# Performance work log

Hardware: AMD Instinct MI355X
Metric: run time of the kernel (lower is better)

Reference implementation:

```python
import jax, jax.numpy as jnp
import numpy as np

EPS = 1e-5
CURVE_LEN = 16


def gather_neighbors(feature, idx):
    # feature: [B, C, N], idx: [B, N, k] -> [B, C, N, k]
    return jax.vmap(lambda f, i: f[:, i])(feature, idx)


def cloud_walk(feature, knn_idx):
    # feature: [B, C, N], knn_idx: [B, N, k] -> walk_index [B, N, 16] (int)
    B, C, N = feature.shape
    neigh = gather_neighbors(feature, knn_idx)                 # [B, C, N, k]
    sim = jnp.einsum('bcn,bcnk->bnk', feature, neigh)          # [B, N, k]
    attn = jax.nn.softmax(sim, axis=-1)
    top4 = jax.lax.top_k(attn, 4)[1]                           # [B, N, 4]
    tmp = top4.reshape(B * N, 4)
    nxt = top4[:, :, 1]                                        # [B, N]
    walks = [nxt]
    for _ in range(CURVE_LEN - 1):
        # faithful to original: index rows of tmp by previous step's values
        nxt = tmp[nxt.reshape(-1), 1].reshape(B, N)
        walks.append(nxt)
    return jnp.stack(walks, axis=-1)                           # [B, N, 16]


def self_attention_layer(feature, walk_idx, Wq, bq, Wk, bk, Wv, bv, gamma, beta):
    # feature: [B, C, N], walk_idx: [B, N, 16]
    wf = gather_neighbors(feature, walk_idx)                   # [B, C, N, 16]
    wf = jnp.transpose(wf, (0, 2, 3, 1))                       # [B, N, 16, C]
    center = jnp.transpose(feature, (0, 2, 1))[:, :, None, :]  # [B, N, 1, C]
    win = jnp.concatenate([wf, center], axis=2)                # [B, N, 17, C]
    Q = win @ Wq.T + bq
    K = win @ Wk.T + bk
    V = win @ Wv.T + bv
    sim = jnp.einsum('bnic,bnjc->bnij', Q, K)                  # [B, N, 17, 17]
    attn = jax.nn.softmax(sim, axis=-1)
    # original einsum 'bnkk,bnkc->bnc' => diagonal of attention weights V
    d = jnp.diagonal(attn, axis1=2, axis2=3)                   # [B, N, 17]
    out = jnp.einsum('bnk,bnkc->bnc', d, V)                    # [B, N, C]
    x = jnp.transpose(out, (0, 2, 1))                          # [B, C, N]
    # BatchNorm1d, training mode: stats over (batch, points), biased variance
    mean = jnp.mean(x, axis=(0, 2), keepdims=True)
    var = jnp.mean((x - mean) ** 2, axis=(0, 2), keepdims=True)
    x = gamma[None, :, None] * (x - mean) / jnp.sqrt(var + EPS) + beta[None, :, None]
    x = jax.nn.relu(x)
    return feature + x


def setup_inputs() -> dict:
    key = jax.random.key(0)
    B, C, N, k = 2, 64, 32768, 16
    ks = jax.random.split(key, 10)
    feature = jax.random.normal(ks[0], (B, C, N), dtype=jnp.float32)
    knn_idx = jax.random.randint(ks[1], (B, N, k), 0, N)
    Wq = jax.random.normal(ks[2], (3, C, C), dtype=jnp.float32) * 0.05
    bq = jax.random.normal(ks[3], (3, C), dtype=jnp.float32) * 0.05
    Wk = jax.random.normal(ks[4], (3, C, C), dtype=jnp.float32) * 0.05
    bk = jax.random.normal(ks[5], (3, C), dtype=jnp.float32) * 0.05
    Wv = jax.random.normal(ks[6], (3, C, C), dtype=jnp.float32) * 0.05
    bv = jax.random.normal(ks[7], (3, C), dtype=jnp.float32) * 0.05
    gamma = jnp.ones((3, C), dtype=jnp.float32)
    beta = jnp.zeros((3, C), dtype=jnp.float32)
    return {"feature": feature, "knn_idx": knn_idx, "Wq": Wq, "bq": bq,
            "Wk": Wk, "bk": bk, "Wv": Wv, "bv": bv, "gamma": gamma, "beta": beta}


def reference(feature, knn_idx, Wq, bq, Wk, bk, Wv, bv, gamma, beta):
    walk_idx = cloud_walk(feature, knn_idx)
    heads = []
    f = feature
    for i in range(3):
        f = self_attention_layer(f, walk_idx, Wq[i], bq[i], Wk[i], bk[i],
                                 Wv[i], bv[i], gamma[i], beta[i])
        heads.append(f)
    return jnp.concatenate(heads, axis=1)  # [B, 3C, N]
```

## Files before the change

kernel.cpp:

```cpp
#include <hip/hip_runtime.h>
#include <math.h>

#define NB 2
#define NC 64
#define NN 32768
#define NPTS (NB*NN)
#define NWAVES 1056
#define NSLOTS 67584

typedef _Float16 half_t;
typedef _Float16 f16x8 __attribute__((ext_vector_type(8)));
typedef _Float16 f16x4 __attribute__((ext_vector_type(4)));
typedef float f32x4 __attribute__((ext_vector_type(4)));

__global__ void k_transpose(const float* __restrict__ f, float* __restrict__ fT,
                            half_t* __restrict__ xh) {
    int blk = blockIdx.x;
    int b = blk / (NN/64);
    int n0 = (blk % (NN/64)) * 64;
    __shared__ float tile[64][65];
    int t = threadIdx.x;
    int dn = t & 63, c0 = t >> 6;
    for (int i = 0; i < 16; ++i) {
        int c = c0 + i*4;
        tile[c][dn] = f[((size_t)(b*NC + c))*NN + n0 + dn];
    }
    __syncthreads();
    int o = t & 63, d0 = t >> 6;
    for (int i = 0; i < 16; ++i) {
        int dn2 = d0 + i*4;
        size_t idx = ((size_t)(b*NN + n0 + dn2))*64 + o;
        float v = tile[o][dn2];
        fT[idx] = v;
        xh[idx] = (half_t)v;
    }
}

__global__ __launch_bounds__(256, 4) void k_s2(const float* __restrict__ fT,
                                               const int* __restrict__ knn,
                                               int* __restrict__ s2buf) {
    int t = threadIdx.x;
    int gp = blockIdx.x * 16 + (t >> 4);
    int l16 = t & 15;
    int q4 = l16 & 3;
    int h4 = l16 >> 2;
    int b = gp >> 15;
    const float4* cen4 = (const float4*)(fT + (size_t)gp*64 + q4*16);
    float4 c0 = cen4[0], c1 = cen4[1], c2 = cen4[2], c3 = cen4[3];
    float own[4];
    #pragma unroll
    for (int kk = 0; kk < 4; ++kk) {
        int idx = knn[(gp << 4) + h4*4 + kk];
        const float4* nb = (const float4*)(fT + ((size_t)(b*NN + idx))*64 + q4*16);
        float4 n0 = nb[0], n1 = nb[1], n2 = nb[2], n3 = nb[3];
        double a = 0.0;
        a += (double)c0.x*(double)n0.x + (double)c0.y*(double)n0.y
           + (double)c0.z*(double)n0.z + (double)c0.w*(double)n0.w;
        a += (double)c1.x*(double)n1.x + (double)c1.y*(double)n1.y
           + (double)c1.z*(double)n1.z + (double)c1.w*(double)n1.w;
        a += (double)c2.x*(double)n2.x + (double)c2.y*(double)n2.y
           + (double)c2.z*(double)n2.z + (double)c2.w*(double)n2.w;
        a += (double)c3.x*(double)n3.x + (double)c3.y*(double)n3.y
           + (double)c3.z*(double)n3.z + (double)c3.w*(double)n3.w;
        a += __shfl_xor(a, 1, 64);
        a += __shfl_xor(a, 2, 64);
        own[kk] = (float)a;
    }
    int base16 = t & 48;
    float sims[16];
    #pragma unroll
    for (int j = 0; j < 16; ++j)
        sims[j] = __shfl(own[j & 3], base16 + ((j >> 2) << 2), 64);
    float m = sims[0];
    #pragma unroll
    for (int k = 1; k < 16; ++k) m = fmaxf(m, sims[k]);
    float e[16]; float Z = 0.f;
    #pragma unroll
    for (int k = 0; k < 16; ++k) { e[k] = expf(sims[k]-m); Z += e[k]; }
    float b1 = -1.f, b2 = -1.f; int i1 = -1, i2 = -1;
    #pragma unroll
    for (int k = 0; k < 16; ++k) {
        float a = e[k]/Z;
        if (a > b1)      { b2 = b1; i2 = i1; b1 = a; i1 = k; }
        else if (a > b2) { b2 = a; i2 = k; }
    }
    if (l16 == 0) s2buf[gp] = i2;
}

__global__ void k_hist2(const int* __restrict__ s2buf, int* __restrict__ bh) {
    __shared__ int hst[32];
    int t = threadIdx.x, blk = blockIdx.x;
    if (t < 32) hst[t] = 0;
    __syncthreads();
    int p = blk*256 + t;
    int bucket = (p >> 15)*16 + s2buf[p];
    atomicAdd(&hst[bucket], 1);
    __syncthreads();
    if (t < 32) bh[t*256 + blk] = hst[t];
}

__global__ void k_prefix(const int* __restrict__ s2buf, const int* __restrict__ bh,
                         int* __restrict__ blockoff, int* __restrict__ wavebucket,
                         int* __restrict__ slotlist, int* __restrict__ walkrows) {
    __shared__ int tot[32], wst[32], offsh;
    __shared__ int T[16];
    int t = threadIdx.x;
    if (t < 16) T[t] = s2buf[t];
    if (t < 32) {
        int s = 0;
        for (int b = 0; b < 256; ++b) s += bh[t*256 + b];
        tot[t] = s;
    }
    __syncthreads();
    if (t < 16) {
        int w = t;
        walkrows[t*16 + 0] = w;
        for (int s = 1; s < 16; ++s) { w = T[w]; walkrows[t*16 + s] = w; }
    }
    if (t == 0) {
        int off = 0;
        for (int i = 0; i < 32; ++i) {
            wst[i] = off;
            off += ((tot[i] + 63) >> 6) << 6;
        }
        offsh = off;
    }
    __syncthreads();
    if (t < 32) {
        int run = wst[t];
        for (int b = 0; b < 256; ++b) {
            blockoff[t*256 + b] = run;
            run += bh[t*256 + b];
        }
        int w0 = wst[t] >> 6, nw = (tot[t] + 63) >> 6;
        for (int w = 0; w < nw; ++w) wavebucket[w0 + w] = t;
        for (int s = wst[t] + tot[t]; s < wst[t] + nw*64; ++s) slotlist[s] = -1;
    }
    __syncthreads();
    int off = offsh;
    for (int w = (off >> 6) + t; w < NWAVES; w += 256) wavebucket[w] = -1;
    for (int s = off + t; s < NSLOTS; s += 256) slotlist[s] = -1;
}

__global__ void k_scatter2(const int* __restrict__ s2buf,
                           const int* __restrict__ blockoff,
                           int* __restrict__ slotlist) {
    __shared__ int hst[32], base[32];
    int t = threadIdx.x, blk = blockIdx.x;
    if (t < 32) { hst[t] = 0; base[t] = blockoff[t*256 + blk]; }
    __syncthreads();
    int p = blk*256 + t;
    int bucket = (p >> 15)*16 + s2buf[p];
    int r = atomicAdd(&hst[bucket], 1);
    slotlist[base[bucket] + r] = p;
}

__global__ __launch_bounds__(256) void k_precomp(
        const float* __restrict__ fT,
        const float* __restrict__ Wq, const float* __restrict__ bq,
        const float* __restrict__ Wk, const float* __restrict__ bk,
        const float* __restrict__ Wv, const float* __restrict__ bv,
        const int* __restrict__ walkrows,
        half_t* __restrict__ Pq16, half_t* __restrict__ Pk16,
        half_t* __restrict__ PvT16, float* __restrict__ Pstat,
        half_t* __restrict__ wh) {
    int blk = blockIdx.x;
    int b = blk >> 4, sv = blk & 15;
    size_t bsv16 = (size_t)(b*16 + sv) * 1024;
    int bs48 = (b*16 + sv)*48;
    __shared__ float win[16][64];
    __shared__ float Wl[64][65];
    __shared__ float qw[16][65], kw[16][65];
    __shared__ float simw[16][17];
    __shared__ int wr[16];
    int t = threadIdx.x;
    #pragma unroll
    for (int j = 0; j < 2; ++j) {
        int idx = j*8192 + blk*256 + t;
        if (idx < 12288) {
            float v = idx < 4096 ? Wq[idx] : (idx < 8192 ? Wk[idx-4096] : Wv[idx-8192]);
            wh[idx] = (half_t)v;
        }
    }
    if (t < 16) wr[t] = walkrows[sv*16 + t];
    __syncthreads();
    #pragma unroll
    for (int i = 0; i < 4; ++i) {
        int idx = t + i*256; int tt = idx >> 6, c = idx & 63;
        win[tt][c] = fT[((size_t)(b*NN + wr[tt]))*64 + c];
    }
    int wv = t >> 6, lane = t & 63;
    for (int m = 0; m < 3; ++m) {
        const float* W  = m == 0 ? Wq : (m == 1 ? Wk : Wv);
        const float* bb = m == 0 ? bq : (m == 1 ? bk : bv);
        __syncthreads();
        #pragma unroll
        for (int i = 0; i < 16; ++i) {
            int idx = t + i*256;
            Wl[idx >> 6][idx & 63] = W[idx];
        }
        __syncthreads();
        float acc[4] = {0.f, 0.f, 0.f, 0.f};
        for (int c = 0; c < 64; ++c) {
            float w_ = Wl[lane][c];
            #pragma unroll
            for (int r = 0; r < 4; ++r) acc[r] = fmaf(w_, win[wv*4 + r][c], acc[r]);
        }
        float bias = bb[lane];
        #pragma unroll
        for (int r = 0; r < 4; ++r) {
            int tt = wv*4 + r;
            float val = acc[r] + bias;
            if (m == 0)      { qw[tt][lane] = val; Pq16[bsv16 + tt*64 + lane] = (half_t)val; }
            else if (m == 1) { kw[tt][lane] = val; Pk16[bsv16 + tt*64 + lane] = (half_t)val; }
            else             {                     PvT16[bsv16 + lane*16 + tt] = (half_t)val; }
        }
    }
    __syncthreads();
    {
        int i = t >> 4, j = t & 15;
        float acc = 0.f;
        for (int o = 0; o < 64; ++o) acc = fmaf(qw[i][o], kw[j][o], acc);
        simw[i][j] = acc;
    }
    __syncthreads();
    if (t < 16) {
        float mx = simw[t][0];
        for (int j = 1; j < 16; ++j) mx = fmaxf(mx, simw[t][j]);
        float z = 0.f;
        for (int j = 0; j < 16; ++j) z += expf(simw[t][j] - mx);
        Pstat[bs48 + t*3 + 0] = mx;
        Pstat[bs48 + t*3 + 1] = z;
        Pstat[bs48 + t*3 + 2] = simw[t][t];
    }
}

__global__ __launch_bounds__(256) void k_gemm(
        const half_t* __restrict__ xh, const int* __restrict__ slotlist, int s0,
        const half_t* __restrict__ wh,
        const float* __restrict__ bq, const float* __restrict__ bk,
        const float* __restrict__ bv,
        half_t* __restrict__ qh, half_t* __restrict__ kh, half_t* __restrict__ vh) {
    __shared__ __align__(16) half_t XO[256*72];
    __shared__ __align__(16) half_t WL[192*72];
    int t = threadIdx.x;
    int lane = t & 63, wv = t >> 6;
    size_t go = (size_t)blockIdx.x * 256 * 64;
    {
        int srow = slotlist[s0 + blockIdx.x*256 + t];
        int prow = srow < 0 ? 0 : srow;
        const uint4* src = (const uint4*)(xh + (size_t)prow*64);
        #pragma unroll
        for (int j = 0; j < 8; ++j) *(uint4*)&XO[t*72 + j*8] = src[j];
    }
    #pragma unroll
    for (int j = 0; j < 6; ++j) {
        int idx8 = t + j*256;
        int row = idx8 >> 3, c0 = (idx8 & 7) * 8;
        *(uint4*)&WL[row*72 + c0] = *(const uint4*)(wh + idx8*8);
    }
    __syncthreads();
    int m15 = lane & 15, k0 = (lane >> 4) * 8;
    int ar = wv*64 + m15;
    f16x8 a00 = *(const f16x8*)&XO[(ar    )*72 + k0];
    f16x8 a01 = *(const f16x8*)&XO[(ar    )*72 + k0 + 32];
    f16x8 a10 = *(const f16x8*)&XO[(ar+16)*72 + k0];
    f16x8 a11 = *(const f16x8*)&XO[(ar+16)*72 + k0 + 32];
    f16x8 a20 = *(const f16x8*)&XO[(ar+32)*72 + k0];
    f16x8 a21 = *(const f16x8*)&XO[(ar+32)*72 + k0 + 32];
    f16x8 a30 = *(const f16x8*)&XO[(ar+48)*72 + k0];
    f16x8 a31 = *(const f16x8*)&XO[(ar+48)*72 + k0 + 32];
    __syncthreads();
    #pragma unroll 1
    for (int m = 0; m < 3; ++m) {
        const float* bias = m == 0 ? bq : (m == 1 ? bk : bv);
        half_t* outp      = m == 0 ? qh : (m == 1 ? kh : vh);
        int wb = m*64 + m15;
        f16x8 b00 = *(const f16x8*)&WL[(wb    )*72 + k0];
        f16x8 b01 = *(const f16x8*)&WL[(wb    )*72 + k0 + 32];
        f16x8 b10 = *(const f16x8*)&WL[(wb+16)*72 + k0];
        f16x8 b11 = *(const f16x8*)&WL[(wb+16)*72 + k0 + 32];
        f16x8 b20 = *(const f16x8*)&WL[(wb+32)*72 + k0];
        f16x8 b21 = *(const f16x8*)&WL[(wb+32)*72 + k0 + 32];
        f16x8 b30 = *(const f16x8*)&WL[(wb+48)*72 + k0];
        f16x8 b31 = *(const f16x8*)&WL[(wb+48)*72 + k0 + 32];
        float bs0 = bias[m15], bs1 = bias[16+m15], bs2 = bias[32+m15], bs3 = bias[48+m15];
        f32x4 Z = {0.f, 0.f, 0.f, 0.f};
        f32x4 c00=Z,c01=Z,c02=Z,c03=Z, c10=Z,c11=Z,c12=Z,c13=Z;
        f32x4 c20=Z,c21=Z,c22=Z,c23=Z, c30=Z,c31=Z,c32=Z,c33=Z;
        #define MM(i,j) \
            c##i##j = __builtin_amdgcn_mfma_f32_16x16x32_f16(a##i##0, b##j##0, c##i##j, 0,0,0); \
            c##i##j = __builtin_amdgcn_mfma_f32_16x16x32_f16(a##i##1, b##j##1, c##i##j, 0,0,0);
        MM(0,0) MM(0,1) MM(0,2) MM(0,3)
        MM(1,0) MM(1,1) MM(1,2) MM(1,3)
        MM(2,0) MM(2,1) MM(2,2) MM(2,3)
        MM(3,0) MM(3,1) MM(3,2) MM(3,3)
        #undef MM
        __syncthreads();
        int r0 = wv*64 + ((lane >> 4) << 2);
        #define WR(i,j,bsj) { \
            XO[(r0 + i*16 + 0)*64 + j*16 + m15] = (half_t)(c##i##j[0] + bsj); \
            XO[(r0 + i*16 + 1)*64 + j*16 + m15] = (half_t)(c##i##j[1] + bsj); \
            XO[(r0 + i*16 + 2)*64 + j*16 + m15] = (half_t)(c##i##j[2] + bsj); \
            XO[(r0 + i*16 + 3)*64 + j*16 + m15] = (half_t)(c##i##j[3] + bsj); }
        WR(0,0,bs0) WR(0,1,bs1) WR(0,2,bs2) WR(0,3,bs3)
        WR(1,0,bs0) WR(1,1,bs1) WR(1,2,bs2) WR(1,3,bs3)
        WR(2,0,bs0) WR(2,1,bs1) WR(2,2,bs2) WR(2,3,bs3)
        WR(3,0,bs0) WR(3,1,bs1) WR(3,2,bs2) WR(3,3,bs3)
        #undef WR
        __syncthreads();
        #pragma unroll
        for (int j = 0; j < 8; ++j) {
            int idx = (j*256 + t) * 8;
            *(uint4*)(outp + go + idx) = *(const uint4*)&XO[idx];
        }
    }
}

__global__ __launch_bounds__(256) void k_comb4(
        const half_t* __restrict__ qh, const half_t* __restrict__ kh,
        const half_t* __restrict__ vh,
        const half_t* __restrict__ Pq16, const half_t* __restrict__ Pk16,
        const half_t* __restrict__ PvT16, const float* __restrict__ Pstat,
        const int* __restrict__ slotlist, const int* __restrict__ wavebucket,
        half_t* __restrict__ xo, int s0) {
    int t = threadIdx.x, j = t >> 6, lane = t & 63;
    int wslot = blockIdx.x*64;
    int gbase = s0 + wslot;
    int bucket = wavebucket[gbase >> 6];
    if (bucket < 0) return;
    int m15 = lane & 15, g4 = lane >> 4;
    int k0h = g4 * 8;
    size_t bsv16 = (size_t)bucket << 10;
    int bs48 = bucket * 48;

    f16x8 pqA0 = *(const f16x8*)&Pq16[bsv16 + m15*64 + k0h];
    f16x8 pqA1 = *(const f16x8*)&Pq16[bsv16 + m15*64 + k0h + 32];
    f16x8 pkA0 = *(const f16x8*)&Pk16[bsv16 + m15*64 + k0h];
    f16x8 pkA1 = *(const f16x8*)&Pk16[bsv16 + m15*64 + k0h + 32];
    f16x4 pvB0 = *(const f16x4*)&PvT16[bsv16 + (0*16 + m15)*16 + g4*4];
    f16x4 pvB1 = *(const f16x4*)&PvT16[bsv16 + (1*16 + m15)*16 + g4*4];
    f16x4 pvB2 = *(const f16x4*)&PvT16[bsv16 + (2*16 + m15)*16 + g4*4];
    f16x4 pvB3 = *(const f16x4*)&PvT16[bsv16 + (3*16 + m15)*16 + g4*4];
    float pm[4], pz[4], dg[4];
    #pragma unroll
    for (int r = 0; r < 4; ++r) {
        pm[r] = Pstat[bs48 + (g4*4+r)*3 + 0];
        pz[r] = Pstat[bs48 + (g4*4+r)*3 + 1];
        dg[r] = Pstat[bs48 + (g4*4+r)*3 + 2];
    }
    int4 pid4 = *(const int4*)&slotlist[gbase + j*16 + g4*4];

    const half_t* kp = kh + (size_t)(wslot + j*16 + m15)*64;
    const half_t* qp = qh + (size_t)(wslot + j*16 + m15)*64;
    f16x8 kB0 = *(const f16x8*)&kp[k0h];
    f16x8 kB1 = *(const f16x8*)&kp[k0h + 32];
    f16x8 qB0 = *(const f16x8*)&qp[k0h];
    f16x8 qB1 = *(const f16x8*)&qp[k0h + 32];
    f32x4 Zz = {0.f,0.f,0.f,0.f};
    f32x4 sp = __builtin_amdgcn_mfma_f32_16x16x32_f16(pqA0, kB0, Zz, 0,0,0);
    sp = __builtin_amdgcn_mfma_f32_16x16x32_f16(pqA1, kB1, sp, 0,0,0);
    f32x4 tp = __builtin_amdgcn_mfma_f32_16x16x32_f16(pkA0, qB0, Zz, 0,0,0);
    tp = __builtin_amdgcn_mfma_f32_16x16x32_f16(pkA1, qB1, tp, 0,0,0);
    float up = 0.f;
    #pragma unroll
    for (int e = 0; e < 8; ++e) {
        up = fmaf((float)qB0[e], (float)kB0[e], up);
        up = fmaf((float)qB1[e], (float)kB1[e], up);
    }
    up += __shfl_xor(up, 16, 64);
    up += __shfl_xor(up, 32, 64);
    float d0, d1, d2, d3;
    {
        float mi, zi;
        mi = fmaxf(pm[0], sp[0]); zi = pz[0]*expf(pm[0]-mi) + expf(sp[0]-mi); d0 = expf(dg[0]-mi)/zi;
        mi = fmaxf(pm[1], sp[1]); zi = pz[1]*expf(pm[1]-mi) + expf(sp[1]-mi); d1 = expf(dg[1]-mi)/zi;
        mi = fmaxf(pm[2], sp[2]); zi = pz[2]*expf(pm[2]-mi) + expf(sp[2]-mi); d2 = expf(dg[2]-mi)/zi;
        mi = fmaxf(pm[3], sp[3]); zi = pz[3]*expf(pm[3]-mi) + expf(sp[3]-mi); d3 = expf(dg[3]-mi)/zi;
    }
    float tmax = fmaxf(fmaxf(tp[0], tp[1]), fmaxf(tp[2], tp[3]));
    tmax = fmaxf(tmax, __shfl_xor(tmax, 16, 64));
    tmax = fmaxf(tmax, __shfl_xor(tmax, 32, 64));
    float mc = fmaxf(tmax, up);
    float ze = expf(tp[0]-mc) + expf(tp[1]-mc) + expf(tp[2]-mc) + expf(tp[3]-mc);
    ze += __shfl_xor(ze, 16, 64);
    ze += __shfl_xor(ze, 32, 64);
    float ec = expf(up - mc);
    float dcen = ec / (ze + ec);
    f16x4 dA; dA[0] = (half_t)d0; dA[1] = (half_t)d1; dA[2] = (half_t)d2; dA[3] = (half_t)d3;

    float dc0 = __shfl(dcen, g4*4 + 0, 64);
    float dc1 = __shfl(dcen, g4*4 + 1, 64);
    float dc2 = __shfl(dcen, g4*4 + 2, 64);
    float dc3 = __shfl(dcen, g4*4 + 3, 64);
    int p0 = pid4.x, p1 = pid4.y, p2 = pid4.z, p3 = pid4.w;
    size_t vb0 = (size_t)(wslot + j*16 + g4*4 + 0)*64;
    size_t vb1 = (size_t)(wslot + j*16 + g4*4 + 1)*64;
    size_t vb2 = (size_t)(wslot + j*16 + g4*4 + 2)*64;
    size_t vb3 = (size_t)(wslot + j*16 + g4*4 + 3)*64;
    #pragma unroll
    for (int jc = 0; jc < 4; ++jc) {
        f16x4 pvB = jc == 0 ? pvB0 : (jc == 1 ? pvB1 : (jc == 2 ? pvB2 : pvB3));
        f32x4 Z2 = {0.f,0.f,0.f,0.f};
        f32x4 acc = __builtin_amdgcn_mfma_f32_16x16x16f16(dA, pvB, Z2, 0,0,0);
        int c = jc*16 + m15;
        float v0 = (float)vh[vb0 + c];
        float v1 = (float)vh[vb1 + c];
        float v2 = (float)vh[vb2 + c];
        float v3 = (float)vh[vb3 + c];
        if (p0 >= 0) xo[(size_t)p0*64 + c] = (half_t)(acc[0] + dc0*v0);
        if (p1 >= 0) xo[(size_t)p1*64 + c] = (half_t)(acc[1] + dc1*v1);
        if (p2 >= 0) xo[(size_t)p2*64 + c] = (half_t)(acc[2] + dc2*v2);
        if (p3 >= 0) xo[(size_t)p3*64 + c] = (half_t)(acc[3] + dc3*v3);
    }
}

__global__ __launch_bounds__(256) void k_reduce(const half_t* __restrict__ x,
                                                float* __restrict__ part) {
    __shared__ float ls[4][64], lq[4][64];
    int t = threadIdx.x, q = t >> 6, c = t & 63;
    size_t base = ((size_t)blockIdx.x*128 + q*32) * 64;
    float s = 0.f, sq = 0.f;
    for (int r = 0; r < 32; ++r) {
        float v = (float)x[base + r*64 + c];
        s += v; sq = fmaf(v, v, sq);
    }
    ls[q][c] = s; lq[q][c] = sq;
    __syncthreads();
    if (q == 0) {
        float S = ls[0][c] + ls[1][c] + ls[2][c] + ls[3][c];
        float Q = lq[0][c] + lq[1][c] + lq[2][c] + lq[3][c];
        part[blockIdx.x*64 + c] = S;
        part[512*64 + blockIdx.x*64 + c] = Q;
    }
}

__global__ __launch_bounds__(256) void k_stats(const float* __restrict__ part,
                                               float* __restrict__ mv) {
    __shared__ float ls[4][64], lq[4][64];
    int t = threadIdx.x, q = t >> 6, c = t & 63;
    float s = 0.f, sq = 0.f;
    for (int r = q*128; r < q*128 + 128; ++r) {
        s  += part[r*64 + c];
        sq += part[512*64 + r*64 + c];
    }
    ls[q][c] = s; lq[q][c] = sq;
    __syncthreads();
    if (q == 0) {
        float S = ls[0][c] + ls[1][c] + ls[2][c] + ls[3][c];
        float Q = lq[0][c] + lq[1][c] + lq[2][c] + lq[3][c];
        float mean = S / (float)NPTS;
        float var  = Q / (float)NPTS - mean*mean;
        mv[c] = mean; mv[64 + c] = var;
    }
}

__global__ void k_norm(const half_t* __restrict__ x, float* __restrict__ fT,
                       const float* __restrict__ mv,
                       const float* __restrict__ gamma, const float* __restrict__ beta,
                       float* __restrict__ out, int l, half_t* __restrict__ xh) {
    int blk = blockIdx.x;
    int b = blk / (NN/64);
    int n0 = (blk % (NN/64)) * 64;
    __shared__ float tile[64][65];
    int t = threadIdx.x;
    int c = t & 63, d0 = t >> 6;
    float mean = mv[c], var = mv[64+c];
    float inv = 1.0f / sqrtf(var + 1e-5f);
    float ga = gamma[c], be = beta[c];
    for (int i = 0; i < 16; ++i) {
        int dn = d0 + i*4;
        size_t pi = ((size_t)(b*NN + n0 + dn))*64 + c;
        float xv = (float)x[pi];
        float y = fT[pi] + fmaxf(ga * (xv - mean) * inv + be, 0.f);
        fT[pi] = y;
        xh[pi] = (half_t)y;
        tile[dn][c] = y;
    }
    __syncthreads();
    int dn2 = t & 63, c0 = t >> 6;
    for (int i = 0; i < 16; ++i) {
        int cc = c0 + i*4;
        out[((size_t)(b*192 + l*64 + cc))*NN + n0 + dn2] = tile[dn2][cc];
    }
}

extern "C" void kernel_launch(void* const* d_in, const int* in_sizes, int n_in,
                              void* d_out, int out_size, void* d_ws, size_t ws_size,
                              hipStream_t stream) {
    const float* feature = (const float*)d_in[0];
    const int*   knn     = (const int*)d_in[1];
    const float* Wq = (const float*)d_in[2];
    const float* bq = (const float*)d_in[3];
    const float* Wk = (const float*)d_in[4];
    const float* bk = (const float*)d_in[5];
    const float* Wv = (const float*)d_in[6];
    const float* bv = (const float*)d_in[7];
    const float* gamma = (const float*)d_in[8];
    const float* beta  = (const float*)d_in[9];
    float* out = (float*)d_out;

    char* ws = (char*)d_ws;
    float*  fT    = (float*) ws;
    half_t* xh    = (half_t*)(ws + 16777216);
    half_t* xo    = (half_t*)(ws + 25165824);
    int*    s2buf = (int*)   (ws + 33554432);
    int*    walkrows = (int*)(ws + 33816576);
    half_t* Pq16  = (half_t*)(ws + 33817600);
    half_t* Pk16  = (half_t*)(ws + 33883136);
    half_t* PvT16 = (half_t*)(ws + 33948672);
    float*  Pstat = (float*) (ws + 34014208);
    float*  part  = (float*) (ws + 34020352);
    float*  mv    = (float*) (ws + 34282496);
    half_t* wh    = (half_t*)(ws + 34283008);
    int*    bh        = (int*)(ws + 34307584);
    int*    blockoff  = (int*)(ws + 34340352);
    int*    wavebucket= (int*)(ws + 34373120);
    int*    slotlist  = (int*)(ws + 34377344);
    size_t  qkv_off = 34647680;

    size_t avail = ws_size > qkv_off ? ws_size - qkv_off : 0;
    size_t chunk = avail / 384;
    chunk = (chunk / 256) * 256;
    if (chunk > (size_t)NSLOTS) chunk = NSLOTS;
    if (chunk < 256) chunk = 256;
    half_t* qh = (half_t*)(ws + qkv_off);
    half_t* kh = qh + chunk*64;
    half_t* vh = kh + chunk*64;

    k_transpose<<<NB*(NN/64), 256, 0, stream>>>(feature, fT, xh);
    k_s2<<<NPTS/16, 256, 0, stream>>>(fT, knn, s2buf);
    k_hist2<<<NPTS/256, 256, 0, stream>>>(s2buf, bh);
    k_prefix<<<1, 256, 0, stream>>>(s2buf, bh, blockoff, wavebucket, slotlist, walkrows);
    k_scatter2<<<NPTS/256, 256, 0, stream>>>(s2buf, blockoff, slotlist);

    for (int l = 0; l < 3; ++l) {
        k_precomp<<<32, 256, 0, stream>>>(fT, Wq + l*4096, bq + l*64,
                                          Wk + l*4096, bk + l*64,
                                          Wv + l*4096, bv + l*64,
                                          walkrows, Pq16, Pk16, PvT16, Pstat, wh);
        for (size_t s0 = 0; s0 < NSLOTS; s0 += chunk) {
            size_t cn = (s0 + chunk <= NSLOTS) ? chunk : (NSLOTS - s0);
            k_gemm<<<(unsigned)(cn/256), 256, 0, stream>>>(xh, slotlist, (int)s0, wh,
                                                           bq + l*64, bk + l*64, bv + l*64,
                                                           qh, kh, vh);
            k_comb4<<<(unsigned)(cn/64), 256, 0, stream>>>(qh, kh, vh,
                                                           Pq16, Pk16, PvT16, Pstat,
                                                           slotlist, wavebucket,
                                                           xo, (int)s0);
        }
        k_reduce<<<512, 256, 0, stream>>>(xo, part);
        k_stats<<<1, 256, 0, stream>>>(part, mv);
        k_norm<<<NB*(NN/64), 256, 0, stream>>>(xo, fT, mv, gamma + l*64, beta + l*64,
                                               out, l, xh);
    }
}
```

Measured before the change: 219.7 us.

## Fuse BN stats into reduce via last-block atomic and drop fp32 residual

Merges k_stats into the partial-sum reduction kernel: the last block to finish, found through an atomic counter, computes mean and variance, which removes three kernel launches. The residual stream is now kept only in fp16 (xh), so k_norm no longer reads and writes the fp32 fT buffer and k_precomp gathers from xh. This cuts memory traffic in k_norm but accumulates residual values in half precision across the three layers, which lowers accuracy. The counter is reset by the last block, which relies on threadfence ordering.

```diff
diff --git a/kernel.cpp b/kernel.cpp
--- a/kernel.cpp
+++ b/kernel.cpp
@@ -101,10 +101,12 @@
 
 __global__ void k_prefix(const int* __restrict__ s2buf, const int* __restrict__ bh,
                          int* __restrict__ blockoff, int* __restrict__ wavebucket,
-                         int* __restrict__ slotlist, int* __restrict__ walkrows) {
+                         int* __restrict__ slotlist, int* __restrict__ walkrows,
+                         int* __restrict__ cnt) {
     __shared__ int tot[32], wst[32], offsh;
     __shared__ int T[16];
     int t = threadIdx.x;
+    if (t == 0) *cnt = 0;
     if (t < 16) T[t] = s2buf[t];
     if (t < 32) {
         int s = 0;
@@ -156,7 +158,7 @@
 }
 
 __global__ __launch_bounds__(256) void k_precomp(
-        const float* __restrict__ fT,
+        const half_t* __restrict__ xh,
         const float* __restrict__ Wq, const float* __restrict__ bq,
         const float* __restrict__ Wk, const float* __restrict__ bk,
         const float* __restrict__ Wv, const float* __restrict__ bv,
@@ -187,7 +189,7 @@
     #pragma unroll
     for (int i = 0; i < 4; ++i) {
         int idx = t + i*256; int tt = idx >> 6, c = idx & 63;
-        win[tt][c] = fT[((size_t)(b*NN + wr[tt]))*64 + c];
+        win[tt][c] = (float)xh[((size_t)(b*NN + wr[tt]))*64 + c];
     }
     int wv = t >> 6, lane = t & 63;
     for (int m = 0; m < 3; ++m) {
@@ -415,9 +417,12 @@
     }
 }
 
-__global__ __launch_bounds__(256) void k_reduce(const half_t* __restrict__ x,
-                                                float* __restrict__ part) {
+__global__ __launch_bounds__(256) void k_reduce2(const half_t* __restrict__ x,
+                                                 float* __restrict__ part,
+                                                 float* __restrict__ mv,
+                                                 int* __restrict__ cnt) {
     __shared__ float ls[4][64], lq[4][64];
+    __shared__ int lastf;
     int t = threadIdx.x, q = t >> 6, c = t & 63;
     size_t base = ((size_t)blockIdx.x*128 + q*32) * 64;
     float s = 0.f, sq = 0.f;
@@ -433,18 +438,22 @@
         part[blockIdx.x*64 + c] = S;
         part[512*64 + blockIdx.x*64 + c] = Q;
     }
-}
-
-__global__ __launch_bounds__(256) void k_stats(const float* __restrict__ part,
-                                               float* __restrict__ mv) {
-    __shared__ float ls[4][64], lq[4][64];
-    int t = threadIdx.x, q = t >> 6, c = t & 63;
-    float s = 0.f, sq = 0.f;
+    __syncthreads();
+    if (t == 0) {
+        __threadfence();
+        int old = atomicAdd(cnt, 1);
+        lastf = (old == 511);
+    }
+    __syncthreads();
+    if (!lastf) return;
+    __threadfence();
+    float s2 = 0.f, sq2 = 0.f;
     for (int r = q*128; r < q*128 + 128; ++r) {
-        s  += part[r*64 + c];
-        sq += part[512*64 + r*64 + c];
-    }
-    ls[q][c] = s; lq[q][c] = sq;
+        s2  += part[r*64 + c];
+        sq2 += part[512*64 + r*64 + c];
+    }
+    __syncthreads();
+    ls[q][c] = s2; lq[q][c] = sq2;
     __syncthreads();
     if (q == 0) {
         float S = ls[0][c] + ls[1][c] + ls[2][c] + ls[3][c];
@@ -453,12 +462,13 @@
         float var  = Q / (float)NPTS - mean*mean;
         mv[c] = mean; mv[64 + c] = var;
     }
-}
-
-__global__ void k_norm(const half_t* __restrict__ x, float* __restrict__ fT,
+    if (t == 0) atomicExch(cnt, 0);
+}
+
+__global__ void k_norm(const half_t* __restrict__ x, half_t* __restrict__ xh,
                        const float* __restrict__ mv,
                        const float* __restrict__ gamma, const float* __restrict__ beta,
-                       float* __restrict__ out, int l, half_t* __restrict__ xh) {
+                       float* __restrict__ out, int l) {
     int blk = blockIdx.x;
     int b = blk / (NN/64);
     int n0 = (blk % (NN/64)) * 64;
@@ -472,8 +482,8 @@
         int dn = d0 + i*4;
         size_t pi = ((size_t)(b*NN + n0 + dn))*64 + c;
         float xv = (float)x[pi];
-        float y = fT[pi] + fmaxf(ga * (xv - mean) * inv + be, 0.f);
-        fT[pi] = y;
+        float res = (float)xh[pi];
+        float y = res + fmaxf(ga * (xv - mean) * inv + be, 0.f);
         xh[pi] = (half_t)y;
         tile[dn][c] = y;
     }
@@ -517,7 +527,8 @@
     int*    blockoff  = (int*)(ws + 34340352);
     int*    wavebucket= (int*)(ws + 34373120);
     int*    slotlist  = (int*)(ws + 34377344);
-    size_t  qkv_off = 34647680;
+    int*    cnt       = (int*)(ws + 34647680);
+    size_t  qkv_off = 34647936;
 
     size_t avail = ws_size > qkv_off ? ws_size - qkv_off : 0;
     size_t chunk = avail / 384;
@@ -531,11 +542,12 @@
     k_transpose<<<NB*(NN/64), 256, 0, stream>>>(feature, fT, xh);
     k_s2<<<NPTS/16, 256, 0, stream>>>(fT, knn, s2buf);
     k_hist2<<<NPTS/256, 256, 0, stream>>>(s2buf, bh);
-    k_prefix<<<1, 256, 0, stream>>>(s2buf, bh, blockoff, wavebucket, slotlist, walkrows);
+    k_prefix<<<1, 256, 0, stream>>>(s2buf, bh, blockoff, wavebucket, slotlist,
+                                    walkrows, cnt);
     k_scatter2<<<NPTS/256, 256, 0, stream>>>(s2buf, blockoff, slotlist);
 
     for (int l = 0; l < 3; ++l) {
-        k_precomp<<<32, 256, 0, stream>>>(fT, Wq + l*4096, bq + l*64,
+        k_precomp<<<32, 256, 0, stream>>>(xh, Wq + l*4096, bq + l*64,
                                           Wk + l*4096, bk + l*64,
                                           Wv + l*4096, bv + l*64,
                                           walkrows, Pq16, Pk16, PvT16, Pstat, wh);
@@ -549,9 +561,8 @@
                                                            slotlist, wavebucket,
                                                            xo, (int)s0);
         }
-        k_reduce<<<512, 256, 0, stream>>>(xo, part);
-        k_stats<<<1, 256, 0, stream>>>(part, mv);
-        k_norm<<<NB*(NN/64), 256, 0, stream>>>(xo, fT, mv, gamma + l*64, beta + l*64,
-                                               out, l, xh);
-    }
-}
+        k_reduce2<<<512, 256, 0, stream>>>(xo, part, mv, cnt);
+        k_norm<<<NB*(NN/64), 256, 0, stream>>>(xo, xh, mv, gamma + l*64, beta + l*64,
+                                               out, l);
+    }
+}
```

Result: slower. 238.3 us (+8.5%).
